# Optimization experiments

Measured on AMD Instinct MI355X. Metric: run time of the kernel, lower is better.

## Reference

```python
import jax, jax.numpy as jnp
import numpy as np

D = 1024
K = 3  # depthwise conv kernel size, causal (left pad K-1)


def setup_inputs() -> dict:
    key = jax.random.key(0)
    ks = jax.random.split(key, 6)
    B, L = 16, 2048
    x = jax.random.normal(ks[0], (B, L, D), dtype=jnp.float32)
    s_in = 1.0 / np.sqrt(D)
    Win = jax.random.uniform(ks[1], (3 * D, D), minval=-s_in, maxval=s_in, dtype=jnp.float32)
    bin_ = jax.random.uniform(ks[2], (3 * D,), minval=-s_in, maxval=s_in, dtype=jnp.float32)
    # depthwise Conv1d weight (D, 1, K) -> stored as (D, K)
    s_c = 1.0 / np.sqrt(K)  # fan_in = in_channels/groups * K = K
    wconv = jax.random.uniform(ks[3], (D, K), minval=-s_c, maxval=s_c, dtype=jnp.float32)
    Wout = jax.random.uniform(ks[4], (D, D), minval=-s_in, maxval=s_in, dtype=jnp.float32)
    bout = jax.random.uniform(ks[5], (D,), minval=-s_in, maxval=s_in, dtype=jnp.float32)
    return {"x": x, "Win": Win, "bin_": bin_, "wconv": wconv, "Wout": Wout, "bout": bout}


def reference(x, Win, bin_, wconv, Wout, bout):
    # x: (B, L, D). in_proj -> (B, L, 3D); chunk along channel dim == last dim here
    BCx = jnp.einsum('bld,ed->ble', x, Win) + bin_
    Bg, Cg, xg = jnp.split(BCx, 3, axis=-1)  # each (B, L, D)
    Bx = Bg * xg
    L = Bx.shape[1]
    # causal depthwise conv: pad K-1 zeros on the left of time axis
    xp = jnp.pad(Bx, ((0, 0), (K - 1, 0), (0, 0)))
    conv_out = (wconv[:, 0] * xp[:, 0:L]
                + wconv[:, 1] * xp[:, 1:L + 1]
                + wconv[:, 2] * xp[:, 2:L + 2])  # (B, L, D)
    y = Cg * conv_out
    return jnp.einsum('bld,ed->ble', y, Wout) + bout
```

## Files before the change

### kernel.cpp

```cpp
#include <hip/hip_runtime.h>
#include <hip/hip_bf16.h>

#define D_    1024
#define LSEQ  2048
#define M_    32768
#define K_    1024
#define NT    16

typedef __bf16 bf16x8 __attribute__((ext_vector_type(8)));
typedef float  f32x4  __attribute__((ext_vector_type(4)));

__device__ __forceinline__ unsigned short f2bf(float f) {
  unsigned u = __float_as_uint(f);
  u += 0x7FFFu + ((u >> 16) & 1u);
  return (unsigned short)(u >> 16);
}
__device__ __forceinline__ float bf2f(unsigned short h) {
  return __uint_as_float(((unsigned)h) << 16);
}

__device__ __forceinline__ void gload_lds16(const void* g, void* l) {
  __builtin_amdgcn_global_load_lds((const __attribute__((address_space(1))) void*)g,
                                   (__attribute__((address_space(3))) void*)l,
                                   16, 0, 0);
}

#define FENCE() asm volatile("" ::: "memory")
#define RBAR()  do { FENCE(); __builtin_amdgcn_s_barrier(); FENCE(); } while (0)

#define NX4  (M_ * K_ / 4)
#define NW4  (3072 * K_ / 4)
#define NO4  (D_ * K_ / 4)
__global__ __launch_bounds__(256) void cvt_all(const float* __restrict__ x,
                                               const float* __restrict__ Win,
                                               const float* __restrict__ Wout,
                                               unsigned short* __restrict__ x_b,
                                               unsigned short* __restrict__ Win_b,
                                               unsigned short* __restrict__ Wout_b) {
  int i = blockIdx.x * 256 + threadIdx.x;
  const float* src;
  unsigned short* dst;
  int off;
  if (i < NX4)            { src = x;    dst = x_b;    off = i; }
  else if (i < NX4 + NW4) { src = Win;  dst = Win_b;  off = i - NX4; }
  else                    { src = Wout; dst = Wout_b; off = i - NX4 - NW4; }
  float4 v = ((const float4*)src)[off];
  ushort4 o;
  o.x = f2bf(v.x); o.y = f2bf(v.y); o.z = f2bf(v.z); o.w = f2bf(v.w);
  ((ushort4*)dst)[off] = o;
}


#define LDA(mh) do { _Pragma("unroll") \
  for (int f = 0; f < 4; ++f) { \
    const int o = aRow + ((mh) * 4 + f) * 2048; \
    av[f][0] = *(const bf16x8*)(As + o); \
    av[f][1] = *(const bf16x8*)(As + (o ^ 64)); \
  } } while (0)

#define LDB(nh, bb) do { _Pragma("unroll") \
  for (int f = 0; f < 2; ++f) { \
    const int o = bRow + ((nh) * 2 + f) * 2048; \
    bb[f][0] = *(const bf16x8*)(Bs + o); \
    bb[f][1] = *(const bf16x8*)(Bs + (o ^ 64)); \
  } } while (0)

#define MFMA_Q(mh, nh, bb) do { _Pragma("unroll") \
  for (int f = 0; f < 4; ++f) { _Pragma("unroll") \
    for (int gg = 0; gg < 2; ++gg) { \
      f32x4 cacc = acc[(mh) * 4 + f][(nh) * 2 + gg]; \
      cacc = __builtin_amdgcn_mfma_f32_16x16x32_bf16(av[f][0], bb[gg][0], cacc, 0, 0, 0); \
      cacc = __builtin_amdgcn_mfma_f32_16x16x32_bf16(av[f][1], bb[gg][1], cacc, 0, 0, 0); \
      acc[(mh) * 4 + f][(nh) * 2 + gg] = cacc; \
    } } } while (0)

__device__ __forceinline__ void gemm_core256(char* smem,
    const unsigned short* aBase,
    const unsigned short* b0p, const unsigned short* b1p,
    const unsigned short* b2p, const unsigned short* b3p,
    f32x4 acc[8][4]) {
  const int tid  = threadIdx.x;
  const int lane = tid & 63;
  const int wm   = (tid >> 6) >> 2;
  const int wn   = (tid >> 6) & 3;
  const int quad = lane >> 4;
  const int l16  = lane & 15;
  const int swz  = (quad ^ (l16 & 7)) << 4;
  const int aRow = ((wm << 7) + l16) * 128 + swz;
  const int bRow = ((wn << 6) + l16) * 128 + swz;

  auto STAGE = [&](int t) {
    char* lb = smem + ((t & 1) << 16);
    const int k0 = t << 6;
#pragma unroll
    for (int i = 0; i < 4; ++i)
      gload_lds16(aBase + ((long)i << 16) + k0, lb + tid * 16 + i * 8192);
    gload_lds16(b0p + k0, lb + 32768 + tid * 16);
    gload_lds16(b1p + k0, lb + 32768 + tid * 16 + 8192);
    gload_lds16(b2p + k0, lb + 32768 + tid * 16 + 16384);
    gload_lds16(b3p + k0, lb + 32768 + tid * 16 + 24576);
  };

  STAGE(0);
  STAGE(1);
  asm volatile("s_waitcnt vmcnt(8)" ::: "memory");
  RBAR();

  for (int t = 0; t < NT; ++t) {
    const char* As = smem + ((t & 1) << 16);
    const char* Bs = As + 32768;
    bf16x8 av[4][2], b0[2][2], b1[2][2];

    LDA(0); LDB(0, b0);
    RBAR();
    __builtin_amdgcn_s_setprio(1); MFMA_Q(0, 0, b0); __builtin_amdgcn_s_setprio(0);
    RBAR();
    LDB(1, b1);
    RBAR();
    __builtin_amdgcn_s_setprio(1); MFMA_Q(0, 1, b1); __builtin_amdgcn_s_setprio(0);
    RBAR();
    LDA(1);
    RBAR();
    __builtin_amdgcn_s_setprio(1); MFMA_Q(1, 1, b1); __builtin_amdgcn_s_setprio(0);
    RBAR();
    LDB(0, b0);
    RBAR();
    __builtin_amdgcn_s_setprio(1); MFMA_Q(1, 0, b0); __builtin_amdgcn_s_setprio(0);
    RBAR();

    if (t + 2 < NT) {
      STAGE(t + 2);
      asm volatile("s_waitcnt vmcnt(8)" ::: "memory");
      RBAR();
    } else if (t + 2 == NT) {
      asm volatile("s_waitcnt vmcnt(0)" ::: "memory");
      RBAR();
    }
  }
}

__global__ __launch_bounds__(512, 2) void gemm_inproj(const unsigned short* __restrict__ A,
                                                      const unsigned short* __restrict__ Wb,
                                                      const float* __restrict__ bin,
                                                      unsigned short* __restrict__ Bx,
                                                      unsigned short* __restrict__ Cg) {
  __shared__ __align__(16) char smem[131072];

  const int g  = blockIdx.x;
  const int u  = g >> 3;
  const int m0 = ((g & 7) + 8 * (u / 12)) * 256;
  const int c  = u % 12;
  const bool paired = (c < 8);

  const int tid  = threadIdx.x;
  const int lane = tid & 63;
  const int srow = ((tid >> 6) << 3) + (lane >> 3);
  const int sch  = (lane & 7) ^ (lane >> 3);

  const unsigned short* aBase = A + (long)(m0 + srow) * K_ + sch * 8;
  const unsigned short *b0p, *b1p, *b2p, *b3p;
  int n0;
  if (paired) {
    n0  = c * 128;
    b0p = Wb + (long)(n0 + srow) * K_ + sch * 8;
    b1p = b0p + (long)64 * K_;
    b2p = Wb + (long)(2048 + n0 + srow) * K_ + sch * 8;
    b3p = b2p + (long)64 * K_;
  } else {
    n0  = (c - 8) * 256;
    b0p = Wb + (long)(1024 + n0 + srow) * K_ + sch * 8;
    b1p = b0p + (long)64 * K_;
    b2p = b0p + (long)128 * K_;
    b3p = b0p + (long)192 * K_;
  }

  f32x4 acc[8][4] = {};
  gemm_core256(smem, aBase, b0p, b1p, b2p, b3p, acc);

  const int wm = (tid >> 6) >> 2, wn = (tid >> 6) & 3;
  const int quad = lane >> 4, l16 = lane & 15;
  float* tr = (float*)smem;

  float bvv[4];
#pragma unroll
  for (int ni = 0; ni < 4; ++ni) {
    int col = wn * 64 + ni * 16 + l16;
    bvv[ni] = paired ? ((col < 128) ? bin[n0 + col] : bin[2048 + n0 + col - 128])
                     : bin[1024 + n0 + col];
  }

  const int trr   = tid >> 4;
  const int tcc   = tid & 15;
  const int growb = m0 + ((trr >> 4) << 7) + (trr & 15);

#pragma unroll
  for (int mi = 0; mi < 8; ++mi) {
    __syncthreads();
#pragma unroll
    for (int ni = 0; ni < 4; ++ni) {
      int col = wn * 64 + ni * 16 + l16;
      f32x4 v = acc[mi][ni];
#pragma unroll
      for (int r = 0; r < 4; ++r)
        tr[(wm * 16 + quad * 4 + r) * 260 + col] = v[r] + bvv[ni];
    }
    __syncthreads();

    const int grow = growb + mi * 16;
    if (paired) {
#pragma unroll
      for (int j = 0; j < 2; ++j) {
        int cc = tcc * 4 + j * 64;
        f32x4 bg = *(const f32x4*)&tr[trr * 260 + cc];
        f32x4 xg = *(const f32x4*)&tr[trr * 260 + 128 + cc];
        ushort4 o;
        o.x = f2bf(bg[0] * xg[0]); o.y = f2bf(bg[1] * xg[1]);
        o.z = f2bf(bg[2] * xg[2]); o.w = f2bf(bg[3] * xg[3]);
        *(ushort4*)&Bx[(long)grow * D_ + n0 + cc] = o;
      }
    } else {
#pragma unroll
      for (int j = 0; j < 4; ++j) {
        int cc = tcc * 4 + j * 64;
        f32x4 v = *(const f32x4*)&tr[trr * 260 + cc];
        ushort4 o;
        o.x = f2bf(v[0]); o.y = f2bf(v[1]); o.z = f2bf(v[2]); o.w = f2bf(v[3]);
        *(ushort4*)&Cg[(long)grow * D_ + n0 + cc] = o;
      }
    }
  }
}

__global__ __launch_bounds__(256) void conv_mul(const unsigned short* __restrict__ Bx,
                                                const unsigned short* __restrict__ Cg,
                                                const float* __restrict__ wconv,
                                                unsigned short* __restrict__ y) {
  __shared__ float wt[3][D_];
  for (int i = threadIdx.x; i < D_; i += 256) {
    wt[0][i] = wconv[i * 3 + 0];
    wt[1][i] = wconv[i * 3 + 1];
    wt[2][i] = wconv[i * 3 + 2];
  }
  __syncthreads();

  int idx = blockIdx.x * 256 + threadIdx.x;
  int bl  = idx >> 7;
  int d8  = (idx & 127) * 8;
  int l   = bl & (LSEQ - 1);

  typedef unsigned short us8 __attribute__((ext_vector_type(8)));
  us8 zz = {0, 0, 0, 0, 0, 0, 0, 0};
  us8 x0 = *(const us8*)&Bx[(long)bl * D_ + d8];
  us8 x1 = (l >= 1) ? *(const us8*)&Bx[(long)(bl - 1) * D_ + d8] : zz;
  us8 x2 = (l >= 2) ? *(const us8*)&Bx[(long)(bl - 2) * D_ + d8] : zz;
  us8 cg = *(const us8*)&Cg[(long)bl * D_ + d8];

  us8 o;
#pragma unroll
  for (int j = 0; j < 8; ++j) {
    float conv = wt[0][d8 + j] * bf2f(x2[j]) + wt[1][d8 + j] * bf2f(x1[j])
               + wt[2][d8 + j] * bf2f(x0[j]);
    o[j] = f2bf(bf2f(cg[j]) * conv);
  }
  *(us8*)&y[(long)bl * D_ + d8] = o;
}

__global__ __launch_bounds__(512, 2) void gemm_out(const unsigned short* __restrict__ A,
                                                   const unsigned short* __restrict__ Wb,
                                                   const float* __restrict__ bias,
                                                   float* __restrict__ Out) {
  __shared__ __align__(16) char smem[131072];

  const int g  = blockIdx.x;
  const int u  = g >> 3;
  const int m0 = ((g & 7) + 8 * (u >> 2)) * 256;
  const int n0 = (u & 3) * 256;

  const int tid  = threadIdx.x;
  const int lane = tid & 63;
  const int srow = ((tid >> 6) << 3) + (lane >> 3);
  const int sch  = (lane & 7) ^ (lane >> 3);

  const unsigned short* aBase = A + (long)(m0 + srow) * K_ + sch * 8;
  const unsigned short* b0p   = Wb + (long)(n0 + srow) * K_ + sch * 8;

  f32x4 acc[8][4] = {};
  gemm_core256(smem, aBase, b0p, b0p + (long)64 * K_, b0p + (long)128 * K_,
               b0p + (long)192 * K_, acc);

  const int wm = (tid >> 6) >> 2, wn = (tid >> 6) & 3;
  const int quad = lane >> 4, l16 = lane & 15;
  float* tr = (float*)smem;

  float bvv[4];
#pragma unroll
  for (int ni = 0; ni < 4; ++ni)
    bvv[ni] = bias[n0 + wn * 64 + ni * 16 + l16];

  const int trr   = tid >> 4;
  const int tcc   = tid & 15;
  const int growb = m0 + ((trr >> 4) << 7) + (trr & 15);

#pragma unroll
  for (int mi = 0; mi < 8; ++mi) {
    __syncthreads();
#pragma unroll
    for (int ni = 0; ni < 4; ++ni) {
      int col = wn * 64 + ni * 16 + l16;
      f32x4 v = acc[mi][ni];
#pragma unroll
      for (int r = 0; r < 4; ++r)
        tr[(wm * 16 + quad * 4 + r) * 260 + col] = v[r] + bvv[ni];
    }
    __syncthreads();

    const int grow = growb + mi * 16;
#pragma unroll
    for (int j = 0; j < 4; ++j) {
      int cc = tcc * 4 + j * 64;
      *(f32x4*)&Out[(long)grow * D_ + n0 + cc] = *(const f32x4*)&tr[trr * 260 + cc];
    }
  }
}

extern "C" void kernel_launch(void* const* d_in, const int* in_sizes, int n_in,
                              void* d_out, int out_size, void* d_ws, size_t ws_size,
                              hipStream_t stream) {
  const float* x     = (const float*)d_in[0];
  const float* Win   = (const float*)d_in[1];
  const float* bin   = (const float*)d_in[2];
  const float* wconv = (const float*)d_in[3];
  const float* Wout  = (const float*)d_in[4];
  const float* bout  = (const float*)d_in[5];

  char* ws = (char*)d_ws;
  unsigned short* x_b    = (unsigned short*)(ws);
  unsigned short* Win_b  = (unsigned short*)(ws + 67108864);
  unsigned short* Wout_b = (unsigned short*)(ws + 73400320);
  unsigned short* Bx_b   = (unsigned short*)(ws + 75497472);
  unsigned short* Cg_b   = (unsigned short*)(ws + 142606336);
  unsigned short* y_b    = (unsigned short*)(ws + 209715200);

  cvt_all<<<(NX4 + NW4 + NO4) / 256, 256, 0, stream>>>(x, Win, Wout, x_b, Win_b, Wout_b);

  gemm_inproj<<<1536, 512, 0, stream>>>(x_b, Win_b, bin, Bx_b, Cg_b);

  conv_mul<<<(M_ * (D_ / 8)) / 256, 256, 0, stream>>>(Bx_b, Cg_b, wconv, y_b);

  gemm_out<<<512, 512, 0, stream>>>(y_b, Wout_b, bout, (float*)d_out);
}
```

Measured before the change: 567.0 us.

## Reschedule GEMM inner loop to interleave LDS reads with MFMAs and overlap staging

Rewrites the per-K-tile schedule of the shared GEMM core. All B fragments are loaded once per tile and kept in registers, so b0 is no longer reloaded. The second-half A loads are interleaved with the MFMAs of the second quadrant, and the global-to-LDS staging of tile t+2 is issued before the last MFMA quadrant rather than after it. This cuts barriers and LDS traffic and hides load latency behind matrix math, at the cost of more live registers, which could cause spills under launch_bounds(512,2).

```diff
diff --git a/kernel.cpp b/kernel.cpp
--- a/kernel.cpp
+++ b/kernel.cpp
@@ -51,29 +51,6 @@
 }
 
 
-#define LDA(mh) do { _Pragma("unroll") \
-  for (int f = 0; f < 4; ++f) { \
-    const int o = aRow + ((mh) * 4 + f) * 2048; \
-    av[f][0] = *(const bf16x8*)(As + o); \
-    av[f][1] = *(const bf16x8*)(As + (o ^ 64)); \
-  } } while (0)
-
-#define LDB(nh, bb) do { _Pragma("unroll") \
-  for (int f = 0; f < 2; ++f) { \
-    const int o = bRow + ((nh) * 2 + f) * 2048; \
-    bb[f][0] = *(const bf16x8*)(Bs + o); \
-    bb[f][1] = *(const bf16x8*)(Bs + (o ^ 64)); \
-  } } while (0)
-
-#define MFMA_Q(mh, nh, bb) do { _Pragma("unroll") \
-  for (int f = 0; f < 4; ++f) { _Pragma("unroll") \
-    for (int gg = 0; gg < 2; ++gg) { \
-      f32x4 cacc = acc[(mh) * 4 + f][(nh) * 2 + gg]; \
-      cacc = __builtin_amdgcn_mfma_f32_16x16x32_bf16(av[f][0], bb[gg][0], cacc, 0, 0, 0); \
-      cacc = __builtin_amdgcn_mfma_f32_16x16x32_bf16(av[f][1], bb[gg][1], cacc, 0, 0, 0); \
-      acc[(mh) * 4 + f][(nh) * 2 + gg] = cacc; \
-    } } } while (0)
-
 __device__ __forceinline__ void gemm_core256(char* smem,
     const unsigned short* aBase,
     const unsigned short* b0p, const unsigned short* b1p,
@@ -106,30 +83,89 @@
   asm volatile("s_waitcnt vmcnt(8)" ::: "memory");
   RBAR();
 
+  bf16x8 av[4][2], b0[2][2], b1[2][2];
+
   for (int t = 0; t < NT; ++t) {
     const char* As = smem + ((t & 1) << 16);
     const char* Bs = As + 32768;
-    bf16x8 av[4][2], b0[2][2], b1[2][2];
-
-    LDA(0); LDB(0, b0);
+
+#pragma unroll
+    for (int f = 0; f < 2; ++f) {
+      const int o = bRow + f * 2048;
+      b0[f][0] = *(const bf16x8*)(Bs + o);
+      b0[f][1] = *(const bf16x8*)(Bs + (o ^ 64));
+    }
+#pragma unroll
+    for (int f = 0; f < 4; ++f) {
+      const int o = aRow + f * 2048;
+      av[f][0] = *(const bf16x8*)(As + o);
+      av[f][1] = *(const bf16x8*)(As + (o ^ 64));
+    }
+#pragma unroll
+    for (int f = 0; f < 2; ++f) {
+      const int o = bRow + (2 + f) * 2048;
+      b1[f][0] = *(const bf16x8*)(Bs + o);
+      b1[f][1] = *(const bf16x8*)(Bs + (o ^ 64));
+    }
     RBAR();
-    __builtin_amdgcn_s_setprio(1); MFMA_Q(0, 0, b0); __builtin_amdgcn_s_setprio(0);
+
+    __builtin_amdgcn_s_setprio(1);
+#pragma unroll
+    for (int f = 0; f < 4; ++f)
+#pragma unroll
+      for (int gg = 0; gg < 2; ++gg) {
+        f32x4 c = acc[f][gg];
+        c = __builtin_amdgcn_mfma_f32_16x16x32_bf16(av[f][0], b0[gg][0], c, 0, 0, 0);
+        c = __builtin_amdgcn_mfma_f32_16x16x32_bf16(av[f][1], b0[gg][1], c, 0, 0, 0);
+        acc[f][gg] = c;
+      }
+    __builtin_amdgcn_s_setprio(0);
     RBAR();
-    LDB(1, b1);
+
+    __builtin_amdgcn_s_setprio(1);
+#pragma unroll
+    for (int f = 0; f < 4; ++f) {
+#pragma unroll
+      for (int gg = 0; gg < 2; ++gg) {
+        f32x4 c = acc[f][2 + gg];
+        c = __builtin_amdgcn_mfma_f32_16x16x32_bf16(av[f][0], b1[gg][0], c, 0, 0, 0);
+        c = __builtin_amdgcn_mfma_f32_16x16x32_bf16(av[f][1], b1[gg][1], c, 0, 0, 0);
+        acc[f][2 + gg] = c;
+      }
+      const int o = aRow + (4 + f) * 2048;
+      av[f][0] = *(const bf16x8*)(As + o);
+      av[f][1] = *(const bf16x8*)(As + (o ^ 64));
+    }
+    __builtin_amdgcn_s_setprio(0);
     RBAR();
-    __builtin_amdgcn_s_setprio(1); MFMA_Q(0, 1, b1); __builtin_amdgcn_s_setprio(0);
+
+    __builtin_amdgcn_s_setprio(1);
+#pragma unroll
+    for (int f = 0; f < 4; ++f)
+#pragma unroll
+      for (int gg = 0; gg < 2; ++gg) {
+        f32x4 c = acc[4 + f][2 + gg];
+        c = __builtin_amdgcn_mfma_f32_16x16x32_bf16(av[f][0], b1[gg][0], c, 0, 0, 0);
+        c = __builtin_amdgcn_mfma_f32_16x16x32_bf16(av[f][1], b1[gg][1], c, 0, 0, 0);
+        acc[4 + f][2 + gg] = c;
+      }
+    __builtin_amdgcn_s_setprio(0);
     RBAR();
-    LDA(1);
-    RBAR();
-    __builtin_amdgcn_s_setprio(1); MFMA_Q(1, 1, b1); __builtin_amdgcn_s_setprio(0);
-    RBAR();
-    LDB(0, b0);
-    RBAR();
-    __builtin_amdgcn_s_setprio(1); MFMA_Q(1, 0, b0); __builtin_amdgcn_s_setprio(0);
-    RBAR();
+
+    if (t + 2 < NT) STAGE(t + 2);
+    __builtin_amdgcn_s_setprio(1);
+#pragma unroll
+    for (int f = 0; f < 4; ++f)
+#pragma unroll
+      for (int gg = 0; gg < 2; ++gg) {
+        f32x4 c = acc[4 + f][gg];
+        c = __builtin_amdgcn_mfma_f32_16x16x32_bf16(av[f][0], b0[gg][0], c, 0, 0, 0);
+        c = __builtin_amdgcn_mfma_f32_16x16x32_bf16(av[f][1], b0[gg][1], c, 0, 0, 0);
+        acc[4 + f][gg] = c;
+      }
+    __builtin_amdgcn_s_setprio(0);
 
     if (t + 2 < NT) {
-      STAGE(t + 2);
       asm volatile("s_waitcnt vmcnt(8)" ::: "memory");
       RBAR();
     } else if (t + 2 == NT) {
```

New measurement: 546.6 us. -3.6%, faster.
